# Kernel optimization log

Measured on AMD Instinct MI355X. Metric: run time of the kernel, lower is better.

The kernel has to match this reference:

```python
import jax, jax.numpy as jnp
import numpy as np

WIN = 9  # window size per spatial dim (default [9,9,9] for 3D)


def _window_sum(x):
    # Depthwise conv with an all-ones [9,9,9] kernel, stride 1, zero pad 4
    # == sliding-window box sum. lax.reduce_window is the efficient, exact form.
    pad = WIN // 2
    return jax.lax.reduce_window(
        x, 0.0, jax.lax.add,
        window_dimensions=(1, 1, WIN, WIN, WIN),
        window_strides=(1, 1, 1, 1, 1),
        padding=((0, 0), (0, 0), (pad, pad), (pad, pad), (pad, pad)),
    )


def setup_inputs() -> dict:
    key = jax.random.key(0)
    k1, k2 = jax.random.split(key)
    shape = (2, 1, 160, 160, 160)  # [B, C, D, H, W]
    y_true = jax.random.normal(k1, shape, dtype=jnp.float32)
    y_pred = jax.random.normal(k2, shape, dtype=jnp.float32)
    return {"y_true": y_true, "y_pred": y_pred}


def reference(y_true, y_pred):
    Ii, Ji = y_true, y_pred
    win_size = jnp.asarray(WIN ** 3, dtype=Ii.dtype)  # 729

    I2 = Ii * Ii
    J2 = Ji * Ji
    IJ = Ii * Ji

    I_sum = _window_sum(Ii)
    J_sum = _window_sum(Ji)
    I2_sum = _window_sum(I2)
    J2_sum = _window_sum(J2)
    IJ_sum = _window_sum(IJ)

    u_I = I_sum / win_size
    u_J = J_sum / win_size

    cross = IJ_sum - u_J * I_sum - u_I * J_sum + u_I * u_J * win_size
    I_var = I2_sum - 2.0 * u_I * I_sum + u_I * u_I * win_size
    J_var = J2_sum - 2.0 * u_J * J_sum + u_J * u_J * win_size

    cc = cross * cross / (I_var * J_var + 1e-05)
    # mean over spatial dims [2,3,4] -> [B,C], then mean -> scalar
    return (1.0 - jnp.mean(cc, axis=(2, 3, 4))).mean()
```

## Files before the change

kernel.cpp:

```cpp
#include <hip/hip_runtime.h>


typedef float floatx2 __attribute__((ext_vector_type(2)));

constexpr int W = 160, H = 160, D = 160;
constexpr int SLICE = W * H;
constexpr int NVOX  = W * H * D;
constexpr int BATCH = 2;
constexpr int FROW  = 5 * W;
constexpr float RW  = 1.0f / 729.0f;

constexpr int TPB_P = 400;
constexpr int XT    = 80;
constexpr int NXT   = W / XT;
constexpr int CZ    = 32;
constexpr int NCZ   = D / CZ;
constexpr int ZS    = CZ + 8;
constexpr int NBLK_P = BATCH * H * NXT * NCZ;

constexpr int TPB_Y = 256;
constexpr int XGY   = W / 8;
constexpr int CHY   = 2, NCHY = H / CHY;
constexpr int NTH_Y = BATCH * D * NCHY * XGY;
constexpr int NBLK_Y = NTH_Y / TPB_Y;

__device__ inline unsigned int pk4(float a, float b, float c, float d) {
    unsigned int u = 0;
    u = __builtin_amdgcn_cvt_pk_fp8_f32(a, b, u, false);
    u = __builtin_amdgcn_cvt_pk_fp8_f32(c, d, u, true);
    return u;
}
__device__ inline void up8(uint2 v, float* o) {
    floatx2 t;
    t = __builtin_amdgcn_cvt_pk_f32_fp8(v.x, false); o[0] = t[0]; o[1] = t[1];
    t = __builtin_amdgcn_cvt_pk_f32_fp8(v.x, true);  o[2] = t[0]; o[3] = t[1];
    t = __builtin_amdgcn_cvt_pk_f32_fp8(v.y, false); o[4] = t[0]; o[5] = t[1];
    t = __builtin_amdgcn_cvt_pk_f32_fp8(v.y, true);  o[6] = t[0]; o[7] = t[1];
}
__device__ inline unsigned short f2bf(float f) {
    unsigned int u = __builtin_bit_cast(unsigned int, f);
    u += 0x7fffu + ((u >> 16) & 1u);
    return (unsigned short)(u >> 16);
}
__device__ inline unsigned int bfpack2(float lo, float hi) {
    return (unsigned int)f2bf(lo) | ((unsigned int)f2bf(hi) << 16);
}
__device__ inline float bflo(unsigned int u) {
    return __builtin_bit_cast(float, u << 16);
}
__device__ inline float bfhi(unsigned int u) {
    return __builtin_bit_cast(float, u & 0xffff0000u);
}

__global__ __launch_bounds__(TPB_P) void pass_pzx(const float* __restrict__ I,
                                                  const float* __restrict__ J,
                                                  unsigned char* __restrict__ outA) {
    __shared__ unsigned short xw[5][ZS][XT];

    int blk = blockIdx.x;
    int zc = blk % NCZ;
    int xt = (blk / NCZ) % NXT;
    int y  = (blk / (NCZ * NXT)) % H;
    int b  = blk / (NCZ * NXT * H);
    int tx0 = xt * XT;
    int zbase = zc * CZ - 4;
    const float* Ib = I + (size_t)b * NVOX + y * W;
    const float* Jb = J + (size_t)b * NVOX + y * W;

    const float4 Z4 = make_float4(0.f, 0.f, 0.f, 0.f);
    {
        int u = threadIdx.x;
        int zs = u / 10;
        int xu = u % 10;
        int gxs = tx0 + xu * 8;
        int gz = zbase + zs;
        float a[16], c[16];
        if (gz >= 0 && gz < D) {
            const float* ip = Ib + (size_t)gz * SLICE + gxs;
            const float* jp = Jb + (size_t)gz * SLICE + gxs;
            float4 A0 = (gxs >= 4)      ? *(const float4*)(ip - 4) : Z4;
            float4 A1 = *(const float4*)(ip);
            float4 A2 = *(const float4*)(ip + 4);
            float4 A3 = (gxs + 11 < W)  ? *(const float4*)(ip + 8) : Z4;
            float4 C0 = (gxs >= 4)      ? *(const float4*)(jp - 4) : Z4;
            float4 C1 = *(const float4*)(jp);
            float4 C2 = *(const float4*)(jp + 4);
            float4 C3 = (gxs + 11 < W)  ? *(const float4*)(jp + 8) : Z4;
            float at[16] = {A0.x,A0.y,A0.z,A0.w, A1.x,A1.y,A1.z,A1.w,
                            A2.x,A2.y,A2.z,A2.w, A3.x,A3.y,A3.z,A3.w};
            float ct[16] = {C0.x,C0.y,C0.z,C0.w, C1.x,C1.y,C1.z,C1.w,
                            C2.x,C2.y,C2.z,C2.w, C3.x,C3.y,C3.z,C3.w};
#pragma unroll
            for (int k = 0; k < 16; ++k) { a[k] = at[k]; c[k] = ct[k]; }
        } else {
#pragma unroll
            for (int k = 0; k < 16; ++k) { a[k] = 0.f; c[k] = 0.f; }
        }
#pragma unroll
        for (int f = 0; f < 5; ++f) {
            float v[16];
#pragma unroll
            for (int k = 0; k < 16; ++k) {
                float x = a[k], yv = c[k];
                v[k] = (f == 0) ? x : (f == 1) ? yv :
                       (f == 2) ? x * x : (f == 3) ? yv * yv : x * yv;
            }
            float P[16];
            P[0] = v[0];
#pragma unroll
            for (int k = 1; k < 16; ++k) P[k] = P[k - 1] + v[k];
            float w[8];
            w[0] = P[8];
#pragma unroll
            for (int j = 1; j < 8; ++j) w[j] = P[j + 8] - P[j - 1];
            uint2 pk;
            pk.x = bfpack2(w[0], w[1]);
            pk.y = bfpack2(w[2], w[3]);
            uint2 pk2;
            pk2.x = bfpack2(w[4], w[5]);
            pk2.y = bfpack2(w[6], w[7]);
            *(uint2*)&xw[f][zs][xu * 8]     = pk;
            *(uint2*)&xw[f][zs][xu * 8 + 4] = pk2;
        }
    }

    __syncthreads();

    if (threadIdx.x < 320) {
        int xg = threadIdx.x % 20;
        int zl = threadIdx.x / 20;
        int x0l = xg * 4;
        int zo0 = zl * 2;

        float acc[5][4];
#pragma unroll
        for (int f = 0; f < 5; ++f)
#pragma unroll
            for (int i = 0; i < 4; ++i) acc[f][i] = 0.f;

#pragma unroll
        for (int k = 0; k < 9; ++k) {
#pragma unroll
            for (int f = 0; f < 5; ++f) {
                uint2 v = *(const uint2*)&xw[f][zo0 + k][x0l];
                acc[f][0] += bflo(v.x); acc[f][1] += bfhi(v.x);
                acc[f][2] += bflo(v.y); acc[f][3] += bfhi(v.y);
            }
        }

        int gz0 = zc * CZ + zo0;
        unsigned char* op0 = outA + ((size_t)(b * D + gz0) * H + y) * FROW + tx0 + x0l;
#pragma unroll
        for (int f = 0; f < 5; ++f)
            *(unsigned int*)(op0 + f * W) = pk4(acc[f][0], acc[f][1], acc[f][2], acc[f][3]);

#pragma unroll
        for (int f = 0; f < 5; ++f) {
            uint2 ve = *(const uint2*)&xw[f][zo0 + 9][x0l];
            uint2 vl = *(const uint2*)&xw[f][zo0][x0l];
            acc[f][0] += bflo(ve.x) - bflo(vl.x);
            acc[f][1] += bfhi(ve.x) - bfhi(vl.x);
            acc[f][2] += bflo(ve.y) - bflo(vl.y);
            acc[f][3] += bfhi(ve.y) - bfhi(vl.y);
        }
        unsigned char* op1 = op0 + (size_t)H * FROW;
#pragma unroll
        for (int f = 0; f < 5; ++f)
            *(unsigned int*)(op1 + f * W) = pk4(acc[f][0], acc[f][1], acc[f][2], acc[f][3]);
    }
}

__global__ __launch_bounds__(TPB_Y) void pass_y(const unsigned char* __restrict__ A,
                                                double* __restrict__ partials) {
    int tid = threadIdx.x;
    int t = blockIdx.x * TPB_Y + tid;
    int xg = t % XGY;
    int tup = t / XGY;
    int yc = tup % NCHY;
    int z  = (tup / NCHY) % D;
    int b  = tup / (NCHY * D);
    int x0 = xg * 8;
    const unsigned char* __restrict__ base =
        A + (size_t)(b * D + z) * H * FROW + x0;
    int y0 = yc * CHY;

    float s[5][8];
#pragma unroll
    for (int f = 0; f < 5; ++f)
#pragma unroll
        for (int i = 0; i < 8; ++i) s[f][i] = 0.f;

    int ylo = y0 - 4 < 0 ? 0 : y0 - 4;
    int yhi = y0 + 4 > H - 1 ? H - 1 : y0 + 4;
    for (int yy = ylo; yy <= yhi; ++yy) {
        const unsigned char* rp = base + (size_t)yy * FROW;
#pragma unroll
        for (int f = 0; f < 5; ++f) {
            uint2 v = *(const uint2*)(rp + f * W);
            float u[8]; up8(v, u);
#pragma unroll
            for (int i = 0; i < 8; ++i) s[f][i] += u[i];
        }
    }

    double acc = 0.0;
#pragma unroll
    for (int dy = 0; dy < CHY; ++dy) {
        int ye = y0 + dy + 5, yl = y0 + dy - 4;
        bool he = ye < H, hl = yl >= 0;
        uint2 pe[5], pl[5];
        const unsigned char* pre = base + (size_t)(he ? ye : 0) * FROW;
        const unsigned char* prl = base + (size_t)(hl ? yl : 0) * FROW;
#pragma unroll
        for (int f = 0; f < 5; ++f) {
            pe[f] = he ? *(const uint2*)(pre + f * W) : make_uint2(0u, 0u);
            pl[f] = hl ? *(const uint2*)(prl + f * W) : make_uint2(0u, 0u);
        }

        float rowcc = 0.f;
#pragma unroll
        for (int i = 0; i < 8; ++i) {
            float Is = s[0][i], Js = s[1][i];
            float I2s = s[2][i], J2s = s[3][i], IJs = s[4][i];
            float tI = RW * Is;
            float cross = __builtin_fmaf(-tI, Js, IJs);
            float Iv    = __builtin_fmaf(-tI, Is, I2s);
            float Jv    = __builtin_fmaf(-(RW * Js), Js, J2s);
            float den   = __builtin_fmaf(Iv, Jv, 1e-5f);
            rowcc = __builtin_fmaf(cross * cross, __builtin_amdgcn_rcpf(den), rowcc);
        }
        acc += (double)rowcc;

#pragma unroll
        for (int f = 0; f < 5; ++f) {
            float ue[8], ul[8];
            up8(pe[f], ue); up8(pl[f], ul);
#pragma unroll
            for (int i = 0; i < 8; ++i) s[f][i] += ue[i] - ul[i];
        }
    }

#pragma unroll
    for (int off = 32; off > 0; off >>= 1) acc += __shfl_down(acc, off);
    __shared__ double sm[TPB_Y / 64];
    if ((tid & 63) == 0) sm[tid >> 6] = acc;
    __syncthreads();
    if (tid == 0) {
        double tt = 0.0;
#pragma unroll
        for (int i = 0; i < TPB_Y / 64; ++i) tt += sm[i];
        partials[blockIdx.x] = tt;
    }
}

__global__ __launch_bounds__(256) void finalize(const double* __restrict__ p,
                                                float* __restrict__ out) {
    double v = 0.0;
    for (int i = threadIdx.x; i < NBLK_Y; i += 256) v += p[i];
#pragma unroll
    for (int off = 32; off > 0; off >>= 1) v += __shfl_down(v, off);
    __shared__ double sm[4];
    int lane = threadIdx.x & 63, wid = threadIdx.x >> 6;
    if (lane == 0) sm[wid] = v;
    __syncthreads();
    if (threadIdx.x == 0) {
        double tt = 0.0;
#pragma unroll
        for (int i = 0; i < 4; ++i) tt += sm[i];
        out[0] = (float)(1.0 - tt / (double)((double)BATCH * (double)NVOX));
    }
}

extern "C" void kernel_launch(void* const* d_in, const int* in_sizes, int n_in,
                              void* d_out, int out_size, void* d_ws, size_t ws_size,
                              hipStream_t stream) {
    const float* I = (const float*)d_in[0];
    const float* J = (const float*)d_in[1];
    float* out = (float*)d_out;

    size_t bufsz = ((size_t)BATCH * 5 * NVOX + 255) / 256 * 256;
    unsigned char* bufA = (unsigned char*)d_ws;
    double* partials = (double*)(bufA + bufsz);

    pass_pzx<<<NBLK_P, TPB_P, 0, stream>>>(I, J, bufA);
    pass_y<<<NBLK_Y, TPB_Y, 0, stream>>>(bufA, partials);
    finalize<<<1, 256, 0, stream>>>(partials, out);
}
```

Before: 64.08 us.

## Interleave five fp8 feature planes per 8-voxel group and widen z-pass per-thread work

The intermediate fp8 buffer changes from five separate planar rows to one 40-byte record, padded to 48, per 8-voxel x group. This lets the y pass fetch all five features with two 16-byte loads and one 8-byte load instead of five scattered 8-byte loads. The z pass now has each thread handle 8 x-values for a single z output instead of 4 x-values for two z outputs, which drops the sliding update and writes each record with wide stores. The padding adds a fifth to the intermediate traffic, and the y pass now does conditional sequential row loads instead of hoisting them.

```diff
diff --git a/kernel.cpp b/kernel.cpp
--- a/kernel.cpp
+++ b/kernel.cpp
@@ -7,8 +7,11 @@
 constexpr int SLICE = W * H;
 constexpr int NVOX  = W * H * D;
 constexpr int BATCH = 2;
-constexpr int FROW  = 5 * W;
 constexpr float RW  = 1.0f / 729.0f;
+
+constexpr int NG   = W / 8;
+constexpr int GB   = 48;
+constexpr int ROWB = NG * GB;
 
 constexpr int TPB_P = 400;
 constexpr int XT    = 80;
@@ -19,7 +22,7 @@
 constexpr int NBLK_P = BATCH * H * NXT * NCZ;
 
 constexpr int TPB_Y = 256;
-constexpr int XGY   = W / 8;
+constexpr int XGY   = NG;
 constexpr int CHY   = 2, NCHY = H / CHY;
 constexpr int NTH_Y = BATCH * D * NCHY * XGY;
 constexpr int NBLK_Y = NTH_Y / TPB_Y;
@@ -30,12 +33,12 @@
     u = __builtin_amdgcn_cvt_pk_fp8_f32(c, d, u, true);
     return u;
 }
-__device__ inline void up8(uint2 v, float* o) {
+__device__ inline void up8u(unsigned int lo, unsigned int hi, float* o) {
     floatx2 t;
-    t = __builtin_amdgcn_cvt_pk_f32_fp8(v.x, false); o[0] = t[0]; o[1] = t[1];
-    t = __builtin_amdgcn_cvt_pk_f32_fp8(v.x, true);  o[2] = t[0]; o[3] = t[1];
-    t = __builtin_amdgcn_cvt_pk_f32_fp8(v.y, false); o[4] = t[0]; o[5] = t[1];
-    t = __builtin_amdgcn_cvt_pk_f32_fp8(v.y, true);  o[6] = t[0]; o[7] = t[1];
+    t = __builtin_amdgcn_cvt_pk_f32_fp8(lo, false); o[0] = t[0]; o[1] = t[1];
+    t = __builtin_amdgcn_cvt_pk_f32_fp8(lo, true);  o[2] = t[0]; o[3] = t[1];
+    t = __builtin_amdgcn_cvt_pk_f32_fp8(hi, false); o[4] = t[0]; o[5] = t[1];
+    t = __builtin_amdgcn_cvt_pk_f32_fp8(hi, true);  o[6] = t[0]; o[7] = t[1];
 }
 __device__ inline unsigned short f2bf(float f) {
     unsigned int u = __builtin_bit_cast(unsigned int, f);
@@ -78,14 +81,14 @@
         if (gz >= 0 && gz < D) {
             const float* ip = Ib + (size_t)gz * SLICE + gxs;
             const float* jp = Jb + (size_t)gz * SLICE + gxs;
-            float4 A0 = (gxs >= 4)      ? *(const float4*)(ip - 4) : Z4;
+            float4 A0 = (gxs >= 4)     ? *(const float4*)(ip - 4) : Z4;
             float4 A1 = *(const float4*)(ip);
             float4 A2 = *(const float4*)(ip + 4);
-            float4 A3 = (gxs + 11 < W)  ? *(const float4*)(ip + 8) : Z4;
-            float4 C0 = (gxs >= 4)      ? *(const float4*)(jp - 4) : Z4;
+            float4 A3 = (gxs + 11 < W) ? *(const float4*)(ip + 8) : Z4;
+            float4 C0 = (gxs >= 4)     ? *(const float4*)(jp - 4) : Z4;
             float4 C1 = *(const float4*)(jp);
             float4 C2 = *(const float4*)(jp + 4);
-            float4 C3 = (gxs + 11 < W)  ? *(const float4*)(jp + 8) : Z4;
+            float4 C3 = (gxs + 11 < W) ? *(const float4*)(jp + 8) : Z4;
             float at[16] = {A0.x,A0.y,A0.z,A0.w, A1.x,A1.y,A1.z,A1.w,
                             A2.x,A2.y,A2.z,A2.w, A3.x,A3.y,A3.z,A3.w};
             float ct[16] = {C0.x,C0.y,C0.z,C0.w, C1.x,C1.y,C1.z,C1.w,
@@ -113,60 +116,60 @@
             w[0] = P[8];
 #pragma unroll
             for (int j = 1; j < 8; ++j) w[j] = P[j + 8] - P[j - 1];
-            uint2 pk;
+            uint4 pk;
             pk.x = bfpack2(w[0], w[1]);
             pk.y = bfpack2(w[2], w[3]);
-            uint2 pk2;
-            pk2.x = bfpack2(w[4], w[5]);
-            pk2.y = bfpack2(w[6], w[7]);
-            *(uint2*)&xw[f][zs][xu * 8]     = pk;
-            *(uint2*)&xw[f][zs][xu * 8 + 4] = pk2;
+            pk.z = bfpack2(w[4], w[5]);
+            pk.w = bfpack2(w[6], w[7]);
+            *(uint4*)&xw[f][zs][xu * 8] = pk;
         }
     }
 
     __syncthreads();
 
     if (threadIdx.x < 320) {
-        int xg = threadIdx.x % 20;
-        int zl = threadIdx.x / 20;
-        int x0l = xg * 4;
-        int zo0 = zl * 2;
-
-        float acc[5][4];
+        int xu = threadIdx.x % 10;
+        int zl = threadIdx.x / 10;
+        int x0l = xu * 8;
+
+        float acc[5][8];
 #pragma unroll
         for (int f = 0; f < 5; ++f)
 #pragma unroll
-            for (int i = 0; i < 4; ++i) acc[f][i] = 0.f;
+            for (int i = 0; i < 8; ++i) acc[f][i] = 0.f;
 
 #pragma unroll
         for (int k = 0; k < 9; ++k) {
 #pragma unroll
             for (int f = 0; f < 5; ++f) {
-                uint2 v = *(const uint2*)&xw[f][zo0 + k][x0l];
+                uint4 v = *(const uint4*)&xw[f][zl + k][x0l];
                 acc[f][0] += bflo(v.x); acc[f][1] += bfhi(v.x);
                 acc[f][2] += bflo(v.y); acc[f][3] += bfhi(v.y);
+                acc[f][4] += bflo(v.z); acc[f][5] += bfhi(v.z);
+                acc[f][6] += bflo(v.w); acc[f][7] += bfhi(v.w);
             }
         }
 
-        int gz0 = zc * CZ + zo0;
-        unsigned char* op0 = outA + ((size_t)(b * D + gz0) * H + y) * FROW + tx0 + x0l;
-#pragma unroll
-        for (int f = 0; f < 5; ++f)
-            *(unsigned int*)(op0 + f * W) = pk4(acc[f][0], acc[f][1], acc[f][2], acc[f][3]);
-
-#pragma unroll
-        for (int f = 0; f < 5; ++f) {
-            uint2 ve = *(const uint2*)&xw[f][zo0 + 9][x0l];
-            uint2 vl = *(const uint2*)&xw[f][zo0][x0l];
-            acc[f][0] += bflo(ve.x) - bflo(vl.x);
-            acc[f][1] += bfhi(ve.x) - bfhi(vl.x);
-            acc[f][2] += bflo(ve.y) - bflo(vl.y);
-            acc[f][3] += bfhi(ve.y) - bfhi(vl.y);
-        }
-        unsigned char* op1 = op0 + (size_t)H * FROW;
-#pragma unroll
-        for (int f = 0; f < 5; ++f)
-            *(unsigned int*)(op1 + f * W) = pk4(acc[f][0], acc[f][1], acc[f][2], acc[f][3]);
+        int gz = zc * CZ + zl;
+        int xg8 = xt * 10 + xu;
+        unsigned char* op = outA +
+            ((size_t)((b * D + gz) * H + y) * NG + xg8) * GB;
+        uint4 st0;
+        st0.x = pk4(acc[0][0], acc[0][1], acc[0][2], acc[0][3]);
+        st0.y = pk4(acc[0][4], acc[0][5], acc[0][6], acc[0][7]);
+        st0.z = pk4(acc[1][0], acc[1][1], acc[1][2], acc[1][3]);
+        st0.w = pk4(acc[1][4], acc[1][5], acc[1][6], acc[1][7]);
+        uint4 st1;
+        st1.x = pk4(acc[2][0], acc[2][1], acc[2][2], acc[2][3]);
+        st1.y = pk4(acc[2][4], acc[2][5], acc[2][6], acc[2][7]);
+        st1.z = pk4(acc[3][0], acc[3][1], acc[3][2], acc[3][3]);
+        st1.w = pk4(acc[3][4], acc[3][5], acc[3][6], acc[3][7]);
+        uint2 st2;
+        st2.x = pk4(acc[4][0], acc[4][1], acc[4][2], acc[4][3]);
+        st2.y = pk4(acc[4][4], acc[4][5], acc[4][6], acc[4][7]);
+        *(uint4*)(op)      = st0;
+        *(uint4*)(op + 16) = st1;
+        *(uint2*)(op + 32) = st2;
     }
 }
 
@@ -179,9 +182,8 @@
     int yc = tup % NCHY;
     int z  = (tup / NCHY) % D;
     int b  = tup / (NCHY * D);
-    int x0 = xg * 8;
     const unsigned char* __restrict__ base =
-        A + (size_t)(b * D + z) * H * FROW + x0;
+        A + ((size_t)(b * D + z) * H * NG + xg) * GB;
     int y0 = yc * CHY;
 
     float s[5][8];
@@ -189,34 +191,37 @@
     for (int f = 0; f < 5; ++f)
 #pragma unroll
         for (int i = 0; i < 8; ++i) s[f][i] = 0.f;
+
+    auto tapRow = [&](int yy, float sgn) {
+        const unsigned char* rp = base + (size_t)yy * ROWB;
+        uint4 L0 = *(const uint4*)(rp);
+        uint4 L1 = *(const uint4*)(rp + 16);
+        uint2 L2 = *(const uint2*)(rp + 32);
+        float u[8];
+        up8u(L0.x, L0.y, u);
+#pragma unroll
+        for (int i = 0; i < 8; ++i) s[0][i] += sgn * u[i];
+        up8u(L0.z, L0.w, u);
+#pragma unroll
+        for (int i = 0; i < 8; ++i) s[1][i] += sgn * u[i];
+        up8u(L1.x, L1.y, u);
+#pragma unroll
+        for (int i = 0; i < 8; ++i) s[2][i] += sgn * u[i];
+        up8u(L1.z, L1.w, u);
+#pragma unroll
+        for (int i = 0; i < 8; ++i) s[3][i] += sgn * u[i];
+        up8u(L2.x, L2.y, u);
+#pragma unroll
+        for (int i = 0; i < 8; ++i) s[4][i] += sgn * u[i];
+    };
 
     int ylo = y0 - 4 < 0 ? 0 : y0 - 4;
     int yhi = y0 + 4 > H - 1 ? H - 1 : y0 + 4;
-    for (int yy = ylo; yy <= yhi; ++yy) {
-        const unsigned char* rp = base + (size_t)yy * FROW;
-#pragma unroll
-        for (int f = 0; f < 5; ++f) {
-            uint2 v = *(const uint2*)(rp + f * W);
-            float u[8]; up8(v, u);
-#pragma unroll
-            for (int i = 0; i < 8; ++i) s[f][i] += u[i];
-        }
-    }
+    for (int yy = ylo; yy <= yhi; ++yy) tapRow(yy, 1.f);
 
     double acc = 0.0;
 #pragma unroll
     for (int dy = 0; dy < CHY; ++dy) {
-        int ye = y0 + dy + 5, yl = y0 + dy - 4;
-        bool he = ye < H, hl = yl >= 0;
-        uint2 pe[5], pl[5];
-        const unsigned char* pre = base + (size_t)(he ? ye : 0) * FROW;
-        const unsigned char* prl = base + (size_t)(hl ? yl : 0) * FROW;
-#pragma unroll
-        for (int f = 0; f < 5; ++f) {
-            pe[f] = he ? *(const uint2*)(pre + f * W) : make_uint2(0u, 0u);
-            pl[f] = hl ? *(const uint2*)(prl + f * W) : make_uint2(0u, 0u);
-        }
-
         float rowcc = 0.f;
 #pragma unroll
         for (int i = 0; i < 8; ++i) {
@@ -231,13 +236,9 @@
         }
         acc += (double)rowcc;
 
-#pragma unroll
-        for (int f = 0; f < 5; ++f) {
-            float ue[8], ul[8];
-            up8(pe[f], ue); up8(pl[f], ul);
-#pragma unroll
-            for (int i = 0; i < 8; ++i) s[f][i] += ue[i] - ul[i];
-        }
+        int ye = y0 + dy + 5, yl = y0 + dy - 4;
+        if (ye < H) tapRow(ye, 1.f);
+        if (yl >= 0) tapRow(yl, -1.f);
     }
 
 #pragma unroll
@@ -278,7 +279,7 @@
     const float* J = (const float*)d_in[1];
     float* out = (float*)d_out;
 
-    size_t bufsz = ((size_t)BATCH * 5 * NVOX + 255) / 256 * 256;
+    size_t bufsz = ((size_t)BATCH * D * H * NG * GB + 255) / 256 * 256;
     unsigned char* bufA = (unsigned char*)d_ws;
     double* partials = (double*)(bufA + bufsz);
 
```

Result: slower. 67.34 us (+5.1%).

## Enlarge z-chunk per block and store x-window partials as fp8 in LDS

Applied to the files above, without the earlier changes.

Raises the z chunk handled per block from 32 to 80, so the 8-slice halo loaded and x-prefiltered per block is amortized over more output slices. Each thread now slides its z window over four outputs instead of two, and all 400 threads take part. The LDS intermediate switches from bf16 to fp8 so the larger tile fits in shared memory. The risks are fewer blocks (lower occupancy and parallelism), a grid-stride load loop, and precision loss from quantizing x-partial sums to fp8 before the z accumulation.

```diff
diff --git a/kernel.cpp b/kernel.cpp
--- a/kernel.cpp
+++ b/kernel.cpp
@@ -13,9 +13,10 @@
 constexpr int TPB_P = 400;
 constexpr int XT    = 80;
 constexpr int NXT   = W / XT;
-constexpr int CZ    = 32;
+constexpr int CZ    = 80;
 constexpr int NCZ   = D / CZ;
 constexpr int ZS    = CZ + 8;
+constexpr int NUNITS = ZS * 10;
 constexpr int NBLK_P = BATCH * H * NXT * NCZ;
 
 constexpr int TPB_Y = 256;
@@ -30,32 +31,19 @@
     u = __builtin_amdgcn_cvt_pk_fp8_f32(c, d, u, true);
     return u;
 }
+__device__ inline void up4(unsigned int v, float* o) {
+    floatx2 t;
+    t = __builtin_amdgcn_cvt_pk_f32_fp8(v, false); o[0] = t[0]; o[1] = t[1];
+    t = __builtin_amdgcn_cvt_pk_f32_fp8(v, true);  o[2] = t[0]; o[3] = t[1];
+}
 __device__ inline void up8(uint2 v, float* o) {
-    floatx2 t;
-    t = __builtin_amdgcn_cvt_pk_f32_fp8(v.x, false); o[0] = t[0]; o[1] = t[1];
-    t = __builtin_amdgcn_cvt_pk_f32_fp8(v.x, true);  o[2] = t[0]; o[3] = t[1];
-    t = __builtin_amdgcn_cvt_pk_f32_fp8(v.y, false); o[4] = t[0]; o[5] = t[1];
-    t = __builtin_amdgcn_cvt_pk_f32_fp8(v.y, true);  o[6] = t[0]; o[7] = t[1];
-}
-__device__ inline unsigned short f2bf(float f) {
-    unsigned int u = __builtin_bit_cast(unsigned int, f);
-    u += 0x7fffu + ((u >> 16) & 1u);
-    return (unsigned short)(u >> 16);
-}
-__device__ inline unsigned int bfpack2(float lo, float hi) {
-    return (unsigned int)f2bf(lo) | ((unsigned int)f2bf(hi) << 16);
-}
-__device__ inline float bflo(unsigned int u) {
-    return __builtin_bit_cast(float, u << 16);
-}
-__device__ inline float bfhi(unsigned int u) {
-    return __builtin_bit_cast(float, u & 0xffff0000u);
+    up4(v.x, o); up4(v.y, o + 4);
 }
 
 __global__ __launch_bounds__(TPB_P) void pass_pzx(const float* __restrict__ I,
                                                   const float* __restrict__ J,
                                                   unsigned char* __restrict__ outA) {
-    __shared__ unsigned short xw[5][ZS][XT];
+    __shared__ unsigned char xw[5][ZS][XT];
 
     int blk = blockIdx.x;
     int zc = blk % NCZ;
@@ -68,8 +56,7 @@
     const float* Jb = J + (size_t)b * NVOX + y * W;
 
     const float4 Z4 = make_float4(0.f, 0.f, 0.f, 0.f);
-    {
-        int u = threadIdx.x;
+    for (int u = threadIdx.x; u < NUNITS; u += TPB_P) {
         int zs = u / 10;
         int xu = u % 10;
         int gxs = tx0 + xu * 8;
@@ -78,14 +65,14 @@
         if (gz >= 0 && gz < D) {
             const float* ip = Ib + (size_t)gz * SLICE + gxs;
             const float* jp = Jb + (size_t)gz * SLICE + gxs;
-            float4 A0 = (gxs >= 4)      ? *(const float4*)(ip - 4) : Z4;
+            float4 A0 = (gxs >= 4)     ? *(const float4*)(ip - 4) : Z4;
             float4 A1 = *(const float4*)(ip);
             float4 A2 = *(const float4*)(ip + 4);
-            float4 A3 = (gxs + 11 < W)  ? *(const float4*)(ip + 8) : Z4;
-            float4 C0 = (gxs >= 4)      ? *(const float4*)(jp - 4) : Z4;
+            float4 A3 = (gxs + 11 < W) ? *(const float4*)(ip + 8) : Z4;
+            float4 C0 = (gxs >= 4)     ? *(const float4*)(jp - 4) : Z4;
             float4 C1 = *(const float4*)(jp);
             float4 C2 = *(const float4*)(jp + 4);
-            float4 C3 = (gxs + 11 < W)  ? *(const float4*)(jp + 8) : Z4;
+            float4 C3 = (gxs + 11 < W) ? *(const float4*)(jp + 8) : Z4;
             float at[16] = {A0.x,A0.y,A0.z,A0.w, A1.x,A1.y,A1.z,A1.w,
                             A2.x,A2.y,A2.z,A2.w, A3.x,A3.y,A3.z,A3.w};
             float ct[16] = {C0.x,C0.y,C0.z,C0.w, C1.x,C1.y,C1.z,C1.w,
@@ -114,23 +101,19 @@
 #pragma unroll
             for (int j = 1; j < 8; ++j) w[j] = P[j + 8] - P[j - 1];
             uint2 pk;
-            pk.x = bfpack2(w[0], w[1]);
-            pk.y = bfpack2(w[2], w[3]);
-            uint2 pk2;
-            pk2.x = bfpack2(w[4], w[5]);
-            pk2.y = bfpack2(w[6], w[7]);
-            *(uint2*)&xw[f][zs][xu * 8]     = pk;
-            *(uint2*)&xw[f][zs][xu * 8 + 4] = pk2;
+            pk.x = pk4(w[0], w[1], w[2], w[3]);
+            pk.y = pk4(w[4], w[5], w[6], w[7]);
+            *(uint2*)&xw[f][zs][xu * 8] = pk;
         }
     }
 
     __syncthreads();
 
-    if (threadIdx.x < 320) {
+    {
         int xg = threadIdx.x % 20;
         int zl = threadIdx.x / 20;
         int x0l = xg * 4;
-        int zo0 = zl * 2;
+        int zo0 = zl * 4;
 
         float acc[5][4];
 #pragma unroll
@@ -142,31 +125,34 @@
         for (int k = 0; k < 9; ++k) {
 #pragma unroll
             for (int f = 0; f < 5; ++f) {
-                uint2 v = *(const uint2*)&xw[f][zo0 + k][x0l];
-                acc[f][0] += bflo(v.x); acc[f][1] += bfhi(v.x);
-                acc[f][2] += bflo(v.y); acc[f][3] += bfhi(v.y);
+                unsigned int v = *(const unsigned int*)&xw[f][zo0 + k][x0l];
+                float u[4]; up4(v, u);
+                acc[f][0] += u[0]; acc[f][1] += u[1];
+                acc[f][2] += u[2]; acc[f][3] += u[3];
             }
         }
 
         int gz0 = zc * CZ + zo0;
-        unsigned char* op0 = outA + ((size_t)(b * D + gz0) * H + y) * FROW + tx0 + x0l;
-#pragma unroll
-        for (int f = 0; f < 5; ++f)
-            *(unsigned int*)(op0 + f * W) = pk4(acc[f][0], acc[f][1], acc[f][2], acc[f][3]);
-
-#pragma unroll
-        for (int f = 0; f < 5; ++f) {
-            uint2 ve = *(const uint2*)&xw[f][zo0 + 9][x0l];
-            uint2 vl = *(const uint2*)&xw[f][zo0][x0l];
-            acc[f][0] += bflo(ve.x) - bflo(vl.x);
-            acc[f][1] += bfhi(ve.x) - bfhi(vl.x);
-            acc[f][2] += bflo(ve.y) - bflo(vl.y);
-            acc[f][3] += bfhi(ve.y) - bfhi(vl.y);
-        }
-        unsigned char* op1 = op0 + (size_t)H * FROW;
-#pragma unroll
-        for (int f = 0; f < 5; ++f)
-            *(unsigned int*)(op1 + f * W) = pk4(acc[f][0], acc[f][1], acc[f][2], acc[f][3]);
+        unsigned char* op = outA + ((size_t)(b * D + gz0) * H + y) * FROW + tx0 + x0l;
+#pragma unroll
+        for (int q = 0; q < 4; ++q) {
+#pragma unroll
+            for (int f = 0; f < 5; ++f)
+                *(unsigned int*)(op + f * W) =
+                    pk4(acc[f][0], acc[f][1], acc[f][2], acc[f][3]);
+            if (q < 3) {
+#pragma unroll
+                for (int f = 0; f < 5; ++f) {
+                    unsigned int ve = *(const unsigned int*)&xw[f][zo0 + 9 + q][x0l];
+                    unsigned int vl = *(const unsigned int*)&xw[f][zo0 + q][x0l];
+                    float ue[4], ul[4];
+                    up4(ve, ue); up4(vl, ul);
+                    acc[f][0] += ue[0] - ul[0]; acc[f][1] += ue[1] - ul[1];
+                    acc[f][2] += ue[2] - ul[2]; acc[f][3] += ue[3] - ul[3];
+                }
+                op += (size_t)H * FROW;
+            }
+        }
     }
 }
 
```

New measurement: 60.23 us. 1.06x faster.
